# Performance work log

Measured on AMD Instinct MI355X. Metric: run time of the kernel, lower is better.

Reference implementation:

```python
import jax, jax.numpy as jnp
import numpy as np

NUM_HEADS = 16
ROPE_BASE = 10000.0


def _rotate_half(x):
    x1 = x[..., ::2]
    x2 = x[..., 1::2]
    return jnp.stack((-x2, x1), axis=-1).reshape(x.shape)


def _rope_tables(seq_len, head_dim, dtype):
    inv_freq = 1.0 / (ROPE_BASE ** (jnp.arange(0, head_dim, 2, dtype=jnp.float32) / head_dim))
    t = jnp.arange(seq_len, dtype=jnp.float32)
    freqs = jnp.outer(t, inv_freq)            # [S, head_dim//2]
    emb = jnp.concatenate((freqs, freqs), -1)  # [S, head_dim]
    return jnp.cos(emb).astype(dtype), jnp.sin(emb).astype(dtype)


def setup_inputs() -> dict:
    key = jax.random.key(0)
    ks = jax.random.split(key, 5)
    B, S, H = 1, 4096, 1024
    scale = 1.0 / np.sqrt(H)
    return {
        "x": jax.random.normal(ks[0], (B, S, H), jnp.float32),
        "Wq": jax.random.normal(ks[1], (H, H), jnp.float32) * scale,
        "Wk": jax.random.normal(ks[2], (H, H), jnp.float32) * scale,
        "Wv": jax.random.normal(ks[3], (H, H), jnp.float32) * scale,
        "Wo": jax.random.normal(ks[4], (H, H), jnp.float32) * scale,
        "attention_mask": jnp.ones((B, S), jnp.int32),
    }


def reference(x, Wq, Wk, Wv, Wo, attention_mask):
    B, S, H = x.shape
    hd = H // NUM_HEADS

    def split_heads(t):  # [B,S,H] -> [B,nh,S,hd]
        return t.reshape(B, S, NUM_HEADS, hd).transpose(0, 2, 1, 3)

    q = split_heads(x @ Wq)
    k = split_heads(x @ Wk)
    v = split_heads(x @ Wv)

    cos, sin = _rope_tables(S, hd, x.dtype)
    cos = cos[None, None]  # [1,1,S,hd]
    sin = sin[None, None]
    q = q * cos + _rotate_half(q) * sin
    k = k * cos + _rotate_half(k) * sin

    scores = jnp.einsum("bhqd,bhkd->bhqk", q, k) / jnp.sqrt(jnp.asarray(hd, x.dtype))
    mask = attention_mask.reshape(B, 1, 1, S)
    scores = jnp.where(mask == 0, jnp.finfo(x.dtype).min, scores)
    probs = jax.nn.softmax(scores, axis=-1)
    ctx = jnp.einsum("bhqk,bhkd->bhqd", probs, v)
    ctx = ctx.transpose(0, 2, 1, 3).reshape(B, S, H)
    return ctx @ Wo
```

## Files before the change

### kernel.cpp

```cpp
#include <hip/hip_runtime.h>
#include <cstdint>
#include <cstddef>

#define S_LEN 4096
#define NHEADS 16
#define HD 64
#define HDIM 1024

typedef _Float16 f16x8 __attribute__((ext_vector_type(8)));
typedef _Float16 f16x4 __attribute__((ext_vector_type(4)));
typedef __fp16 h16x2 __attribute__((ext_vector_type(2)));
typedef float f32x4 __attribute__((ext_vector_type(4)));
typedef unsigned char uchar;
typedef unsigned int u32;

__device__ __forceinline__ f32x4 mfma16h(f16x8 a, f16x8 b, f32x4 c) {
    return __builtin_amdgcn_mfma_f32_16x16x32_f16(a, b, c, 0, 0, 0);
}
__device__ __forceinline__ void async16(void* lds, const void* g) {
    __builtin_amdgcn_global_load_lds(
        (const __attribute__((address_space(1))) u32*)g,
        (__attribute__((address_space(3))) u32*)lds, 16, 0, 0);
}


__global__ __launch_bounds__(256) void pack_x(const float* __restrict__ X,
                                              uchar* __restrict__ P,
                                              const int* __restrict__ M,
                                              _Float16* __restrict__ FM16)
{
    int id = blockIdx.x * 256 + threadIdx.x;
    int m = id >> 7, g = id & 127;
    int kc = g >> 3, b = g & 7;
    float v[8];
    *(float4*)&v[0] = *(const float4*)&X[(size_t)m * HDIM + kc * 64 + b * 8];
    *(float4*)&v[4] = *(const float4*)&X[(size_t)m * HDIM + kc * 64 + b * 8 + 4];
    __align__(16) _Float16 h[8];
    #pragma unroll
    for (int i = 0; i < 8; i++) h[i] = (_Float16)v[i];
    size_t base = ((size_t)(m * 16 + kc)) * 128 + (size_t)((b ^ (m & 7)) * 16);
    *(uint4*)(P + base) = *(const uint4*)h;
    if (id < S_LEN) {
        int c = id >> 7, k128 = id & 127;
        int w = k128 >> 5, k32 = k128 & 31;
        int q = (k32 >> 2) & 3, kt = k32 >> 4, r = k32 & 3;
        FM16[c * 128 + w * 32 + q * 8 + kt * 4 + r] =
            (_Float16)((M[id] == 0) ? 0.0f : 1.0f);
    }
}

__global__ __launch_bounds__(256) void pack_w4(
    const float* __restrict__ W0, const float* __restrict__ W1,
    const float* __restrict__ W2, const float* __restrict__ W3,
    uchar* __restrict__ P)
{
    int id = blockIdx.x * 256 + threadIdx.x;
    int wsel = id >> 17;
    int lid  = id & 131071;
    int g = lid >> 10, n = lid & 1023;
    int kc = g >> 3, b = g & 7;
    const float* W = (wsel == 0) ? W0 : (wsel == 1) ? W1 : (wsel == 2) ? W2 : W3;
    uchar* dst = P + (size_t)wsel * 2097152;
    float v[8];
    #pragma unroll
    for (int j = 0; j < 8; j++)
        v[j] = W[(size_t)(kc * 64 + b * 8 + j) * HDIM + n];
    __align__(16) _Float16 h[8];
    #pragma unroll
    for (int i = 0; i < 8; i++) h[i] = (_Float16)v[i];
    size_t base = ((size_t)(n * 16 + kc)) * 128 + (size_t)((b ^ (n & 7)) * 16);
    *(uint4*)(dst + base) = *(const uint4*)h;
}

__global__ __launch_bounds__(256) void gemm_f16(
    const uchar* __restrict__ Ap, const uchar* __restrict__ Bp,
    float* __restrict__ C, int head_major)
{
    __shared__ __align__(16) uchar AB[65536];
    const int t = threadIdx.x, lane = t & 63, w = t >> 6;
    const int quad = lane >> 4, l15 = lane & 15, x7 = l15 & 7;
    const int m0 = blockIdx.y * 128, n0 = blockIdx.x * 128;
    const int wm = (w >> 1) * 64, wn = (w & 1) * 64;

    f32x4 acc[4][4];
    const f32x4 zero4 = {0.0f, 0.0f, 0.0f, 0.0f};
    #pragma unroll
    for (int mt = 0; mt < 4; mt++)
        #pragma unroll
        for (int nt = 0; nt < 4; nt++) acc[mt][nt] = zero4;

    #pragma unroll
    for (int i = 0; i < 4; i++) {
        int idx = i * 256 + t;
        int row = idx >> 3, blk = idx & 7;
        int ldso = (idx & ~63) * 16;
        async16(AB + ldso,         Ap + ((size_t)((m0 + row) * 16 + 0)) * 128 + blk * 16);
        async16(AB + 16384 + ldso, Bp + ((size_t)((n0 + row) * 16 + 0)) * 128 + blk * 16);
    }

    for (int kc = 0; kc < 16; kc++) {
        uchar* As = AB + (kc & 1) * 32768;
        uchar* Bs = As + 16384;
        __syncthreads();
        if (kc + 1 < 16) {
            uchar* An = AB + ((kc + 1) & 1) * 32768;
            #pragma unroll
            for (int i = 0; i < 4; i++) {
                int idx = i * 256 + t;
                int row = idx >> 3, blk = idx & 7;
                int ldso = (idx & ~63) * 16;
                async16(An + ldso,
                        Ap + ((size_t)((m0 + row) * 16 + kc + 1)) * 128 + blk * 16);
                async16(An + 16384 + ldso,
                        Bp + ((size_t)((n0 + row) * 16 + kc + 1)) * 128 + blk * 16);
            }
        }
        #pragma unroll
        for (int ks = 0; ks < 2; ks++) {
            const int phys = ((ks * 4 + quad) ^ x7) * 16;
            f16x8 ah[4];
            #pragma unroll
            for (int mt = 0; mt < 4; mt++)
                ah[mt] = *(const f16x8*)(As + (size_t)(wm + mt * 16 + l15) * 128 + phys);
            #pragma unroll
            for (int nt = 0; nt < 4; nt++) {
                f16x8 bh = *(const f16x8*)(Bs + (size_t)(wn + nt * 16 + l15) * 128 + phys);
                #pragma unroll
                for (int mt = 0; mt < 4; mt++)
                    acc[mt][nt] = mfma16h(ah[mt], bh, acc[mt][nt]);
            }
        }
    }

    #pragma unroll
    for (int mt = 0; mt < 4; mt++)
        #pragma unroll
        for (int nt = 0; nt < 4; nt++)
            #pragma unroll
            for (int r = 0; r < 4; r++) {
                int m = m0 + wm + mt * 16 + quad * 4 + r;
                int n = n0 + wn + nt * 16 + l15;
                float val = acc[mt][nt][r];
                if (head_major) {
                    int hh = n >> 6, d = n & 63;
                    C[((size_t)hh * S_LEN + m) * HD + d] = val;
                } else {
                    C[(size_t)m * HDIM + n] = val;
                }
            }
}

__global__ __launch_bounds__(256) void rope_pack(const float* __restrict__ QKVf,
                                                 uchar* __restrict__ Qg,
                                                 uchar* __restrict__ Kg)
{
    int id = blockIdx.x * 256 + threadIdx.x;
    int g  = id & 7;
    int s  = (id >> 3) & (S_LEN - 1);
    int hb = id >> 15;
    const float* src = QKVf + (size_t)hb * (S_LEN * HD) + (size_t)s * HD + g * 8;
    float v[8];
    *(float4*)&v[0] = *(const float4*)&src[0];
    *(float4*)&v[4] = *(const float4*)&src[4];

    const float L32 = 13.287712379549449f / 32.0f;
    float out[8];
    #pragma unroll
    for (int u = 0; u < 4; u++) {
        int de = g * 8 + 2 * u;
        float ae = (float)s * exp2f(-(float)(de & 31) * L32);
        float ao = (float)s * exp2f(-(float)((de + 1) & 31) * L32);
        float ce = __cosf(ae), se = __sinf(ae);
        float co = __cosf(ao), so = __sinf(ao);
        float xe = v[2 * u], xo = v[2 * u + 1];
        out[2 * u]     = xe * ce - xo * se;
        out[2 * u + 1] = xo * co + xe * so;
    }
    const bool isQ = hb < 16;
    const float scale = isQ ? 0.18033688011112042f : 1.0f;
    __align__(16) _Float16 h[8];
    #pragma unroll
    for (int i = 0; i < 8; i++) h[i] = (_Float16)(out[i] * scale);
    uchar* dst = (isQ ? Qg : Kg);
    size_t base = ((size_t)((hb & 15) * S_LEN + s)) * 128 + (size_t)((g ^ (s & 7)) * 16);
    *(uint4*)(dst + base) = *(const uint4*)h;
}

__global__ __launch_bounds__(256) void v_pack(const float* __restrict__ Vf,
                                              const int* __restrict__ M,
                                              uchar* __restrict__ Vg)
{
    int id = blockIdx.x * 256 + threadIdx.x;
    int d    = id & 63;
    int kg   = (id >> 6) & 15;
    int kc2  = (id >> 10) & 31;
    int head = id >> 15;
    __align__(16) _Float16 hv[8];
    #pragma unroll
    for (int j = 0; j < 8; j++) {
        int key = kc2 * 128 + kg * 8 + j;
        float x = Vf[(size_t)head * (S_LEN * HD) + (size_t)key * HD + d];
        hv[j] = (M[key] == 0) ? (_Float16)0.0f : (_Float16)x;
    }
    int wv  = kg >> 2;
    int kgm = kg & 3;
    int kt  = kgm >> 1;
    int qA  = (kgm * 2) & 3;
    int qB  = (kgm * 2 + 1) & 3;
    int slotA = wv * 32 + qA * 8 + kt * 4;
    int slotB = wv * 32 + qB * 8 + kt * 4;
    size_t row = ((size_t)(head * 32 + kc2)) * 16384 + (size_t)d * 256;
    *(ushort4*)(Vg + row + (size_t)(((slotA >> 3) ^ (d & 7)) * 16 + (slotA & 7) * 2))
        = *(const ushort4*)&hv[0];
    *(ushort4*)(Vg + row + (size_t)(((slotB >> 3) ^ (d & 7)) * 16 + (slotB & 7) * 2))
        = *(const ushort4*)&hv[4];
}

#define ISSUE_K(CC, KB)                                                        \
  {                                                                            \
    const uchar* ks_ = kgb + (size_t)(CC) * 16384;                             \
    async16((KB),        ks_ + l16);                                           \
    async16((KB) + 1024, ks_ + 1024 + l16);                                    \
    async16((KB) + 2048, ks_ + 2048 + l16);                                    \
    async16((KB) + 3072, ks_ + 3072 + l16);                                    \
  }
#define ISSUE_V(CC)                                                            \
  {                                                                            \
    const uchar* vs_ = vgb + (size_t)(CC) * 16384;                             \
    async16(VB,        vs_ + voff);                                            \
    async16(VB + 1024, vs_ + 4096 + voff);                                     \
    async16(VB + 2048, vs_ + 8192 + voff);                                     \
    async16(VB + 3072, vs_ + 12288 + voff);                                    \
  }

#define ATTN_STEP(CC, KB, TOPC, MIDC, FLG)                                     \
  {                                                                            \
    asm volatile("s_waitcnt vmcnt(" TOPC ")" ::: "memory");                    \
    f32x4 s0[4], s1[4];                                                        \
    _Pragma("unroll")                                                          \
    for (int qt = 0; qt < 4; qt++) { s0[qt] = zero4; s1[qt] = zero4; }         \
    _Pragma("unroll")                                                          \
    for (int ks = 0; ks < 2; ks++) {                                           \
      const int phys_ = ((ks * 4 + quad) ^ x7) * 16;                           \
      f16x8 kf0 = *(const f16x8*)((KB) + (size_t)l15 * 128 + phys_);           \
      f16x8 kf1 = *(const f16x8*)((KB) + (size_t)(16 + l15) * 128 + phys_);    \
      _Pragma("unroll")                                                        \
      for (int qt = 0; qt < 4; qt++) {                                         \
        s0[qt] = mfma16h(kf0, qf[qt][ks], s0[qt]);                             \
        s1[qt] = mfma16h(kf1, qf[qt][ks], s1[qt]);                             \
      }                                                                        \
    }                                                                          \
    f16x8 pb[4];                                                               \
    _Pragma("unroll")                                                          \
    for (int qt = 0; qt < 4; qt++) {                                           \
      h16x2 c01 = __builtin_amdgcn_cvt_pkrtz(exp2f(s0[qt][0]), exp2f(s0[qt][1])); \
      h16x2 c23 = __builtin_amdgcn_cvt_pkrtz(exp2f(s0[qt][2]), exp2f(s0[qt][3])); \
      h16x2 c45 = __builtin_amdgcn_cvt_pkrtz(exp2f(s1[qt][0]), exp2f(s1[qt][1])); \
      h16x2 c67 = __builtin_amdgcn_cvt_pkrtz(exp2f(s1[qt][2]), exp2f(s1[qt][3])); \
      uint4 pw;                                                                \
      pw.x = __builtin_bit_cast(u32, c01);                                     \
      pw.y = __builtin_bit_cast(u32, c23);                                     \
      pw.z = __builtin_bit_cast(u32, c45);                                     \
      pw.w = __builtin_bit_cast(u32, c67);                                     \
      pb[qt] = __builtin_bit_cast(f16x8, pw);                                  \
    }                                                                          \
    asm volatile("s_waitcnt vmcnt(" MIDC ")" ::: "memory");                    \
    {                                                                          \
      _Pragma("unroll")                                                        \
      for (int dt = 0; dt < 4; dt++) {                                         \
        f16x8 va = *(const f16x8*)(VB + (size_t)(dt * 16 + l15) * 64 + vrd);   \
        _Pragma("unroll")                                                      \
        for (int qt = 0; qt < 4; qt++)                                         \
          o[dt][qt] = mfma16h(va, pb[qt], o[dt][qt]);                          \
      }                                                                        \
      _Pragma("unroll")                                                        \
      for (int qt = 0; qt < 4; qt++)                                           \
        lacc[qt] = mfma16h((FLG), pb[qt], lacc[qt]);                           \
    }                                                                          \
    asm volatile("s_waitcnt lgkmcnt(0)" ::: "memory");                         \
    if ((CC) + 1 < 32) ISSUE_V((CC) + 1);                                      \
    if ((CC) + 2 < 32) {                                                       \
      ISSUE_K((CC) + 2, KB);                                                   \
      (FLG) = *(const f16x8*)(fmw + (size_t)((CC) + 2) * 256);                 \
    }                                                                          \
  }

__global__ __launch_bounds__(256, 2) void attn9(
    const uchar* __restrict__ Qg, const uchar* __restrict__ Kg,
    const uchar* __restrict__ Vg, const uchar* __restrict__ fm16,
    uchar* __restrict__ CTXp)
{
    __shared__ __align__(16) uchar arena[49152];
    __shared__ float Lsh[4][64];
    __shared__ float Lfin[64];
    float* Os = (float*)arena;

    const int t    = threadIdx.x;
    const int lane = t & 63;
    const int w    = t >> 6;
    const int quad = lane >> 4;
    const int l15  = lane & 15;
    const int x7   = l15 & 7;
    const int hh   = blockIdx.y;
    const int m0   = blockIdx.x * 64;

    const uchar* qgb = Qg + (size_t)hh * (S_LEN * 128);
    const uchar* kgb = Kg + (size_t)hh * (S_LEN * 128) + (size_t)w * 4096;
    const uchar* vgb = Vg + (size_t)hh * 32 * 16384;
    const uchar* fmw = fm16 + w * 64 + quad * 16;

    uchar* WB = arena + w * 12288;
    uchar* K0 = WB;
    uchar* K1 = WB + 4096;
    uchar* VB = WB + 8192;

    const int l16 = lane * 16;
    const int vphys = ((w * 4 + ((lane & 3) ^ ((lane >> 2) & 3))) ^ ((lane >> 2) & 7));
    const int voff  = (lane >> 2) * 256 + vphys * 16;
    const int vrd   = (quad ^ (l15 & 3)) * 16;

    f16x8 qf[4][2];
    #pragma unroll
    for (int qt = 0; qt < 4; qt++)
        #pragma unroll
        for (int ks = 0; ks < 2; ks++)
            qf[qt][ks] = *(const f16x8*)(qgb + (size_t)(m0 + qt * 16 + l15) * 128 +
                                         (size_t)(((ks * 4 + quad) ^ x7) * 16));

    f32x4 o[4][4], lacc[4];
    const f32x4 zero4 = {0.0f, 0.0f, 0.0f, 0.0f};
    #pragma unroll
    for (int dt = 0; dt < 4; dt++)
        #pragma unroll
        for (int qt = 0; qt < 4; qt++) o[dt][qt] = zero4;
    #pragma unroll
    for (int qt = 0; qt < 4; qt++) lacc[qt] = zero4;

    ISSUE_K(0, K0);
    ISSUE_V(0);
    f16x8 flagA = *(const f16x8*)(fmw);
    f16x8 flagB = *(const f16x8*)(fmw + 256);
    ISSUE_K(1, K1);

    for (int c = 0; c < 30; c += 2) {
        ATTN_STEP(c,     K0, "8", "4", flagA);
        ATTN_STEP(c + 1, K1, "8", "4", flagB);
    }
    ATTN_STEP(30, K0, "8", "4", flagA);
    ATTN_STEP(31, K1, "4", "0", flagB);

    __syncthreads();
    if (quad == 0) {
        #pragma unroll
        for (int qt = 0; qt < 4; qt++)
            Lsh[w][qt * 16 + l15] = lacc[qt][0];
    }
    __syncthreads();
    if (t < 64)
        Lfin[t] = Lsh[0][t] + Lsh[1][t] + Lsh[2][t] + Lsh[3][t];
    __syncthreads();

    for (int wv = 0; wv < 4; wv++) {
        if (w == wv) {
            #pragma unroll
            for (int dt = 0; dt < 4; dt++)
                #pragma unroll
                for (int qt = 0; qt < 4; qt++)
                    #pragma unroll
                    for (int r = 0; r < 4; r++) {
                        int q = qt * 16 + l15;
                        int d = dt * 16 + quad * 4 + r;
                        float val = o[dt][qt][r];
                        if (wv == 0) Os[q * 68 + d] = val;
                        else         Os[q * 68 + d] += val;
                    }
        }
        __syncthreads();
    }

    #pragma unroll
    for (int i = 0; i < 4; i++) {
        int idx = t + 256 * i;
        int q   = idx >> 4;
        int c4  = (idx & 15) * 4;
        float inv = 1.0f / Lfin[q];
        float4 v = *(const float4*)&Os[q * 68 + c4];
        int m = m0 + q;
        __align__(8) _Float16 h[4];
        h[0] = (_Float16)(v.x * inv);
        h[1] = (_Float16)(v.y * inv);
        h[2] = (_Float16)(v.z * inv);
        h[3] = (_Float16)(v.w * inv);
        size_t base = ((size_t)(m * 16 + hh)) * 128 +
                      (size_t)((((c4 >> 3) ^ (m & 7))) * 16) + (c4 & 7) * 2;
        *(ushort4*)(CTXp + base) = *(const ushort4*)h;
    }
}

extern "C" void kernel_launch(void* const* d_in, const int* in_sizes, int n_in,
                              void* d_out, int out_size, void* d_ws, size_t ws_size,
                              hipStream_t stream)
{
    const float* x   = (const float*)d_in[0];
    const float* Wq  = (const float*)d_in[1];
    const float* Wk  = (const float*)d_in[2];
    const float* Wv  = (const float*)d_in[3];
    const float* Wo  = (const float*)d_in[4];
    const int* amask = (const int*)d_in[5];
    float* out = (float*)d_out;
    float* ws  = (float*)d_ws;

    float* QKVf = ws;
    uchar* Xp   = (uchar*)ws + 50331648;
    uchar* Wt4  = (uchar*)ws + 58720256;
    uchar* Vg   = (uchar*)ws + 67108864;
    _Float16* Fm16 = (_Float16*)((uchar*)ws + 75497472);
    uchar* Qg   = Xp;
    uchar* Kg   = (uchar*)ws + 33554432;
    uchar* CTXp = (uchar*)ws;

    dim3 blk(256);

    pack_x<<<2048, blk, 0, stream>>>(x, Xp, amask, Fm16);
    pack_w4<<<2048, blk, 0, stream>>>(Wq, Wk, Wv, Wo, Wt4);

    gemm_f16<<<dim3(24, 32), blk, 0, stream>>>(Xp, Wt4, QKVf, 1);

    v_pack<<<2048, blk, 0, stream>>>(QKVf + 8388608, amask, Vg);
    rope_pack<<<4096, blk, 0, stream>>>(QKVf, Qg, Kg);

    attn9<<<dim3(S_LEN / 64, NHEADS), blk, 0, stream>>>(Qg, Kg, Vg,
                                                        (const uchar*)Fm16, CTXp);

    gemm_f16<<<dim3(8, 32), blk, 0, stream>>>(CTXp, Wt4 + 6291456, out, 0);
}
```

Before: 249.9 us.

## Single-buffer K in attention loop, reissue K load after QK, use native exp2

Replaces the double-buffered K LDS tiles with a single K buffer per wave. The next chunk's K load is issued right after the QK MFMAs finish reading it, and the vmcnt waits are retuned to match. This cuts LDS from 48KB to 32KB per block, which may allow more resident blocks, but it shortens the prefetch distance for K. It also switches exp2f to the hardware exp2 builtin in both the attention and rope kernels and initialises the QK accumulators directly from zero.

```diff
diff --git a/kernel.cpp b/kernel.cpp
--- a/kernel.cpp
+++ b/kernel.cpp
@@ -168,8 +168,8 @@
     #pragma unroll
     for (int u = 0; u < 4; u++) {
         int de = g * 8 + 2 * u;
-        float ae = (float)s * exp2f(-(float)(de & 31) * L32);
-        float ao = (float)s * exp2f(-(float)((de + 1) & 31) * L32);
+        float ae = (float)s * __builtin_amdgcn_exp2f(-(float)(de & 31) * L32);
+        float ao = (float)s * __builtin_amdgcn_exp2f(-(float)((de + 1) & 31) * L32);
         float ce = __cosf(ae), se = __sinf(ae);
         float co = __cosf(ao), so = __sinf(ao);
         float xe = v[2 * u], xo = v[2 * u + 1];
@@ -216,13 +216,13 @@
         = *(const ushort4*)&hv[4];
 }
 
-#define ISSUE_K(CC, KB)                                                        \
+#define ISSUE_K(CC)                                                            \
   {                                                                            \
     const uchar* ks_ = kgb + (size_t)(CC) * 16384;                             \
-    async16((KB),        ks_ + l16);                                           \
-    async16((KB) + 1024, ks_ + 1024 + l16);                                    \
-    async16((KB) + 2048, ks_ + 2048 + l16);                                    \
-    async16((KB) + 3072, ks_ + 3072 + l16);                                    \
+    async16(KB,        ks_ + l16);                                             \
+    async16(KB + 1024, ks_ + 1024 + l16);                                      \
+    async16(KB + 2048, ks_ + 2048 + l16);                                      \
+    async16(KB + 3072, ks_ + 3072 + l16);                                      \
   }
 #define ISSUE_V(CC)                                                            \
   {                                                                            \
@@ -233,30 +233,41 @@
     async16(VB + 3072, vs_ + 12288 + voff);                                    \
   }
 
-#define ATTN_STEP(CC, KB, TOPC, MIDC, FLG)                                     \
+#define ATTN_STEP(CC, TOPC, MIDC, FLG)                                         \
   {                                                                            \
     asm volatile("s_waitcnt vmcnt(" TOPC ")" ::: "memory");                    \
     f32x4 s0[4], s1[4];                                                        \
-    _Pragma("unroll")                                                          \
-    for (int qt = 0; qt < 4; qt++) { s0[qt] = zero4; s1[qt] = zero4; }         \
-    _Pragma("unroll")                                                          \
-    for (int ks = 0; ks < 2; ks++) {                                           \
-      const int phys_ = ((ks * 4 + quad) ^ x7) * 16;                           \
-      f16x8 kf0 = *(const f16x8*)((KB) + (size_t)l15 * 128 + phys_);           \
-      f16x8 kf1 = *(const f16x8*)((KB) + (size_t)(16 + l15) * 128 + phys_);    \
+    {                                                                          \
+      const int ph0_ = (quad ^ x7) * 16;                                       \
+      f16x8 ka_ = *(const f16x8*)(KB + (size_t)l15 * 128 + ph0_);              \
+      f16x8 kb_ = *(const f16x8*)(KB + (size_t)(16 + l15) * 128 + ph0_);       \
       _Pragma("unroll")                                                        \
       for (int qt = 0; qt < 4; qt++) {                                         \
-        s0[qt] = mfma16h(kf0, qf[qt][ks], s0[qt]);                             \
-        s1[qt] = mfma16h(kf1, qf[qt][ks], s1[qt]);                             \
+        s0[qt] = mfma16h(ka_, qf[qt][0], zero4);                               \
+        s1[qt] = mfma16h(kb_, qf[qt][0], zero4);                               \
+      }                                                                        \
+      const int ph1_ = ((4 + quad) ^ x7) * 16;                                 \
+      f16x8 kc_ = *(const f16x8*)(KB + (size_t)l15 * 128 + ph1_);              \
+      f16x8 kd_ = *(const f16x8*)(KB + (size_t)(16 + l15) * 128 + ph1_);       \
+      _Pragma("unroll")                                                        \
+      for (int qt = 0; qt < 4; qt++) {                                         \
+        s0[qt] = mfma16h(kc_, qf[qt][1], s0[qt]);                              \
+        s1[qt] = mfma16h(kd_, qf[qt][1], s1[qt]);                              \
       }                                                                        \
     }                                                                          \
+    asm volatile("s_waitcnt lgkmcnt(0)" ::: "memory");                         \
+    if ((CC) + 1 < 32) ISSUE_K((CC) + 1);                                      \
     f16x8 pb[4];                                                               \
     _Pragma("unroll")                                                          \
     for (int qt = 0; qt < 4; qt++) {                                           \
-      h16x2 c01 = __builtin_amdgcn_cvt_pkrtz(exp2f(s0[qt][0]), exp2f(s0[qt][1])); \
-      h16x2 c23 = __builtin_amdgcn_cvt_pkrtz(exp2f(s0[qt][2]), exp2f(s0[qt][3])); \
-      h16x2 c45 = __builtin_amdgcn_cvt_pkrtz(exp2f(s1[qt][0]), exp2f(s1[qt][1])); \
-      h16x2 c67 = __builtin_amdgcn_cvt_pkrtz(exp2f(s1[qt][2]), exp2f(s1[qt][3])); \
+      h16x2 c01 = __builtin_amdgcn_cvt_pkrtz(                                  \
+          __builtin_amdgcn_exp2f(s0[qt][0]), __builtin_amdgcn_exp2f(s0[qt][1]));\
+      h16x2 c23 = __builtin_amdgcn_cvt_pkrtz(                                  \
+          __builtin_amdgcn_exp2f(s0[qt][2]), __builtin_amdgcn_exp2f(s0[qt][3]));\
+      h16x2 c45 = __builtin_amdgcn_cvt_pkrtz(                                  \
+          __builtin_amdgcn_exp2f(s1[qt][0]), __builtin_amdgcn_exp2f(s1[qt][1]));\
+      h16x2 c67 = __builtin_amdgcn_cvt_pkrtz(                                  \
+          __builtin_amdgcn_exp2f(s1[qt][2]), __builtin_amdgcn_exp2f(s1[qt][3]));\
       uint4 pw;                                                                \
       pw.x = __builtin_bit_cast(u32, c01);                                     \
       pw.y = __builtin_bit_cast(u32, c23);                                     \
@@ -265,24 +276,19 @@
       pb[qt] = __builtin_bit_cast(f16x8, pw);                                  \
     }                                                                          \
     asm volatile("s_waitcnt vmcnt(" MIDC ")" ::: "memory");                    \
-    {                                                                          \
-      _Pragma("unroll")                                                        \
-      for (int dt = 0; dt < 4; dt++) {                                         \
-        f16x8 va = *(const f16x8*)(VB + (size_t)(dt * 16 + l15) * 64 + vrd);   \
-        _Pragma("unroll")                                                      \
-        for (int qt = 0; qt < 4; qt++)                                         \
-          o[dt][qt] = mfma16h(va, pb[qt], o[dt][qt]);                          \
-      }                                                                        \
+    _Pragma("unroll")                                                          \
+    for (int dt = 0; dt < 4; dt++) {                                           \
+      f16x8 va = *(const f16x8*)(VB + (size_t)(dt * 16 + l15) * 64 + vrd);     \
       _Pragma("unroll")                                                        \
       for (int qt = 0; qt < 4; qt++)                                           \
-        lacc[qt] = mfma16h((FLG), pb[qt], lacc[qt]);                           \
+        o[dt][qt] = mfma16h(va, pb[qt], o[dt][qt]);                            \
     }                                                                          \
+    _Pragma("unroll")                                                          \
+    for (int qt = 0; qt < 4; qt++)                                             \
+      lacc[qt] = mfma16h((FLG), pb[qt], lacc[qt]);                             \
     asm volatile("s_waitcnt lgkmcnt(0)" ::: "memory");                         \
     if ((CC) + 1 < 32) ISSUE_V((CC) + 1);                                      \
-    if ((CC) + 2 < 32) {                                                       \
-      ISSUE_K((CC) + 2, KB);                                                   \
-      (FLG) = *(const f16x8*)(fmw + (size_t)((CC) + 2) * 256);                 \
-    }                                                                          \
+    if ((CC) + 2 < 32) (FLG) = *(const f16x8*)(fmw + (size_t)((CC) + 2) * 256);\
   }
 
 __global__ __launch_bounds__(256, 2) void attn9(
@@ -290,7 +296,7 @@
     const uchar* __restrict__ Vg, const uchar* __restrict__ fm16,
     uchar* __restrict__ CTXp)
 {
-    __shared__ __align__(16) uchar arena[49152];
+    __shared__ __align__(16) uchar arena[32768];
     __shared__ float Lsh[4][64];
     __shared__ float Lfin[64];
     float* Os = (float*)arena;
@@ -309,10 +315,9 @@
     const uchar* vgb = Vg + (size_t)hh * 32 * 16384;
     const uchar* fmw = fm16 + w * 64 + quad * 16;
 
-    uchar* WB = arena + w * 12288;
-    uchar* K0 = WB;
-    uchar* K1 = WB + 4096;
-    uchar* VB = WB + 8192;
+    uchar* WB = arena + w * 8192;
+    uchar* KB = WB;
+    uchar* VB = WB + 4096;
 
     const int l16 = lane * 16;
     const int vphys = ((w * 4 + ((lane & 3) ^ ((lane >> 2) & 3))) ^ ((lane >> 2) & 7));
@@ -336,18 +341,20 @@
     #pragma unroll
     for (int qt = 0; qt < 4; qt++) lacc[qt] = zero4;
 
-    ISSUE_K(0, K0);
-    ISSUE_V(0);
     f16x8 flagA = *(const f16x8*)(fmw);
     f16x8 flagB = *(const f16x8*)(fmw + 256);
-    ISSUE_K(1, K1);
-
-    for (int c = 0; c < 30; c += 2) {
-        ATTN_STEP(c,     K0, "8", "4", flagA);
-        ATTN_STEP(c + 1, K1, "8", "4", flagB);
-    }
-    ATTN_STEP(30, K0, "8", "4", flagA);
-    ATTN_STEP(31, K1, "4", "0", flagB);
+    asm volatile("" ::: "memory");
+    ISSUE_K(0);
+    ISSUE_V(0);
+
+    ATTN_STEP(0, "4", "4", flagA);
+    ATTN_STEP(1, "5", "4", flagB);
+    for (int c = 2; c < 30; c += 2) {
+        ATTN_STEP(c,     "5", "4", flagA);
+        ATTN_STEP(c + 1, "5", "4", flagB);
+    }
+    ATTN_STEP(30, "5", "4", flagA);
+    ATTN_STEP(31, "4", "0", flagB);
 
     __syncthreads();
     if (quad == 0) {
```

Result: faster. 238.3 us (-4.6%).
